# Optimization experiments

Measured on AMD Instinct MI355X. Metric: run time of the kernel, lower is better.

The kernel has to match this reference:

```python
import jax, jax.numpy as jnp
import numpy as np

N = 50000
E = 1600000
F = 128
G = 64  # number of graphs in the batch


def gat_layer(x, src, dst, W, a_src, a_dst, bias, heads, out_dim, concat):
    n = x.shape[0]
    h = (x @ W).reshape(n, heads, out_dim)                      # [N,H,D]
    alpha_src = jnp.sum(h * a_src, axis=-1)                     # [N,H]
    alpha_dst = jnp.sum(h * a_dst, axis=-1)                     # [N,H]
    e = jax.nn.leaky_relu(alpha_src[src] + alpha_dst[dst], negative_slope=0.2)  # [E,H]
    # segment softmax over edges grouped by destination node
    m = jax.ops.segment_max(e, dst, num_segments=n)
    m = jnp.where(jnp.isfinite(m), m, 0.0)
    ex = jnp.exp(e - m[dst])
    denom = jax.ops.segment_sum(ex, dst, num_segments=n)
    alpha = ex / (denom[dst] + 1e-16)                           # [E,H]
    msg = h[src] * alpha[:, :, None]                            # [E,H,D]
    out = jax.ops.segment_sum(msg, dst, num_segments=n)         # [N,H,D]
    if concat:
        out = out.reshape(n, heads * out_dim)
    else:
        out = out.mean(axis=1)
    return out + bias


def setup_inputs() -> dict:
    key = jax.random.key(0)
    ks = jax.random.split(key, 12)
    x = jax.random.normal(ks[0], (N, F), dtype=jnp.float32)
    edge_index = jax.random.randint(ks[1], (2, E), 0, N, dtype=jnp.int32)
    batch = jnp.sort(jax.random.randint(ks[2], (N,), 0, G, dtype=jnp.int32))
    s = 0.1
    W1 = jax.random.normal(ks[3], (F, 4 * 32), dtype=jnp.float32) * s
    a_src1 = jax.random.normal(ks[4], (4, 32), dtype=jnp.float32) * s
    a_dst1 = jax.random.normal(ks[5], (4, 32), dtype=jnp.float32) * s
    b1 = jnp.zeros((4 * 32,), dtype=jnp.float32)
    W2 = jax.random.normal(ks[6], (4 * 32, 2 * 16), dtype=jnp.float32) * s
    a_src2 = jax.random.normal(ks[7], (2, 16), dtype=jnp.float32) * s
    a_dst2 = jax.random.normal(ks[8], (2, 16), dtype=jnp.float32) * s
    b2 = jnp.zeros((16,), dtype=jnp.float32)
    fcW = jax.random.normal(ks[9], (16, 1), dtype=jnp.float32) * s
    fcb = jnp.zeros((1,), dtype=jnp.float32)
    return {"x": x, "edge_index": edge_index, "batch": batch,
            "W1": W1, "a_src1": a_src1, "a_dst1": a_dst1, "b1": b1,
            "W2": W2, "a_src2": a_src2, "a_dst2": a_dst2, "b2": b2,
            "fcW": fcW, "fcb": fcb}


def reference(x, edge_index, batch, W1, a_src1, a_dst1, b1, W2, a_src2, a_dst2, b2, fcW, fcb):
    n = x.shape[0]
    # PyG GATConv default: add self loops
    loops = jnp.arange(n, dtype=edge_index.dtype)
    src = jnp.concatenate([edge_index[0], loops])
    dst = jnp.concatenate([edge_index[1], loops])
    # eval mode: dropouts are no-ops
    h = jax.nn.relu(gat_layer(x, src, dst, W1, a_src1, a_dst1, b1, 4, 32, True))
    h = gat_layer(h, src, dst, W2, a_src2, a_dst2, b2, 2, 16, False)
    # global mean pool over graphs
    sums = jax.ops.segment_sum(h, batch, num_segments=G)        # [G,16]
    counts = jax.ops.segment_sum(jnp.ones((n,), h.dtype), batch, num_segments=G)
    pooled = sums / jnp.maximum(counts, 1.0)[:, None]
    return pooled @ fcW + fcb                                   # [G,1]
```

## Files before the change

kernel.cpp:

```cpp
#include <hip/hip_runtime.h>

#define LRELU(x) ((x) > 0.f ? (x) : 0.2f*(x))
typedef unsigned int uint;
typedef unsigned short ushort;
typedef _Float16 half2_t __attribute__((ext_vector_type(2)));

__device__ inline ushort f2bf(float f) {
    union { float f; unsigned u; } v; v.f = f;
    unsigned r = v.u + 0x7FFF + ((v.u >> 16) & 1);
    return (ushort)(r >> 16);
}
__device__ inline uint packbf(float a, float b) {
    return (uint)f2bf(a) | ((uint)f2bf(b) << 16);
}
__device__ inline float bflo(uint u){ union{uint u; float f;}v; v.u = u<<16; return v.f; }
__device__ inline float bfhi(uint u){ union{uint u; float f;}v; v.u = u & 0xFFFF0000u; return v.f; }
__device__ inline half2_t u2h(uint u){ union{uint u; half2_t h;}v; v.u=u; return v.h; }
__device__ inline uint h2u(half2_t h){ union{half2_t h; uint u;}v; v.h=h; return v.u; }
__device__ inline uint packh(float a, float b){
    half2_t h; h.x = (_Float16)a; h.y = (_Float16)b; return h2u(h);
}


#define CSR_SHIFT 7
#define CSR_NBLK  512

__global__ __launch_bounds__(256) void bucket_count_kernel(
    const int* __restrict__ dst, int E, int chunk, int nb,
    int* __restrict__ blockCntT)
{
    __shared__ int cnt[1024];
    int t = threadIdx.x, k = blockIdx.x;
    for (int i = t; i < nb; i += 256) cnt[i] = 0;
    __syncthreads();
    int e0 = k * chunk, e1 = min(e0 + chunk, E);
    for (int e = e0 + t * 4; e < e1; e += 1024) {
        int4 d4 = *(const int4*)(dst + e);
        atomicAdd(&cnt[d4.x >> CSR_SHIFT], 1);
        atomicAdd(&cnt[d4.y >> CSR_SHIFT], 1);
        atomicAdd(&cnt[d4.z >> CSR_SHIFT], 1);
        atomicAdd(&cnt[d4.w >> CSR_SHIFT], 1);
    }
    __syncthreads();
    for (int b = t; b < nb; b += 256)
        blockCntT[b * CSR_NBLK + k] = cnt[b];
}

__global__ __launch_bounds__(512) void row_scan_kernel(
    int* __restrict__ blockCntT, int* __restrict__ tot)
{
    __shared__ int sm[512];
    int b = blockIdx.x, t = threadIdx.x;
    int* row = blockCntT + b * CSR_NBLK;
    int v = row[t];
    sm[t] = v;
    __syncthreads();
    for (int off = 1; off < 512; off <<= 1) {
        int u = (t >= off) ? sm[t - off] : 0;
        __syncthreads(); sm[t] += u; __syncthreads();
    }
    row[t] = sm[t] - v;
    if (t == 511) tot[b] = sm[511];
}

__global__ __launch_bounds__(1024) void total_scan_kernel(
    const int* __restrict__ tot, int nb, int* __restrict__ bucketBase)
{
    __shared__ int sm[1024];
    int t = threadIdx.x;
    int v = (t < nb) ? tot[t] : 0;
    sm[t] = v;
    __syncthreads();
    for (int off = 1; off < 1024; off <<= 1) {
        int u = (t >= off) ? sm[t - off] : 0;
        __syncthreads(); sm[t] += u; __syncthreads();
    }
    if (t < nb) bucketBase[t] = sm[t] - v;
    if (t == 1023) bucketBase[nb] = sm[1023];
}

__global__ __launch_bounds__(256) void bucket_scatter_kernel(
    const int* __restrict__ src, const int* __restrict__ dst, int E, int chunk, int nb,
    const int* __restrict__ blockCntT, const int* __restrict__ bucketBase,
    uint* __restrict__ ebuf)
{
    __shared__ int cur[1024];
    int t = threadIdx.x, k = blockIdx.x;
    for (int b = t; b < nb; b += 256)
        cur[b] = bucketBase[b] + blockCntT[b * CSR_NBLK + k];
    __syncthreads();
    int e0 = k * chunk, e1 = min(e0 + chunk, E);
    for (int e = e0 + t * 4; e < e1; e += 1024) {
        int4 d4 = *(const int4*)(dst + e);
        int4 s4 = *(const int4*)(src + e);
        int p0 = atomicAdd(&cur[d4.x >> CSR_SHIFT], 1);
        ebuf[p0] = ((uint)s4.x << 7) | (uint)(d4.x & 127);
        int p1 = atomicAdd(&cur[d4.y >> CSR_SHIFT], 1);
        ebuf[p1] = ((uint)s4.y << 7) | (uint)(d4.y & 127);
        int p2 = atomicAdd(&cur[d4.z >> CSR_SHIFT], 1);
        ebuf[p2] = ((uint)s4.z << 7) | (uint)(d4.z & 127);
        int p3 = atomicAdd(&cur[d4.w >> CSR_SHIFT], 1);
        ebuf[p3] = ((uint)s4.w << 7) | (uint)(d4.w & 127);
    }
}

__global__ __launch_bounds__(256) void local_csr_kernel(
    const uint* __restrict__ ebuf, const int* __restrict__ bucketBase,
    int n, int E, int* __restrict__ rowptr, int* __restrict__ csr)
{
    __shared__ int lbase[1 << CSR_SHIFT];
    __shared__ int lcur[1 << CSR_SHIFT];
    __shared__ int ldeg[1 << CSR_SHIFT];
    int b = blockIdx.x, t = threadIdx.x;
    int n0 = b << CSR_SHIFT;
    int base = bucketBase[b], end = bucketBase[b + 1];
    if (t < (1 << CSR_SHIFT)) ldeg[t] = 0;
    __syncthreads();
    for (int e = base + t; e < end; e += 256)
        atomicAdd(&ldeg[ebuf[e] & 127], 1);
    __syncthreads();
    if (t == 0) {
        int run = base;
        for (int i = 0; i < (1 << CSR_SHIFT); ++i) {
            lbase[i] = run; lcur[i] = run; run += ldeg[i];
        }
    }
    __syncthreads();
    int node = n0 + t;
    if (t < (1 << CSR_SHIFT) && node < n) rowptr[node] = lbase[t];
    if (b == 0 && t == 0) rowptr[n] = E;
    for (int e = base + t; e < end; e += 256) {
        uint ed = ebuf[e];
        int pos = atomicAdd(&lcur[ed & 127], 1);
        csr[pos] = (int)(ed >> 7);
    }
}


template<int COLS, int HEADS, bool XBF16>
__global__ __launch_bounds__(256) void gemm_alpha_kernel(
    const void* __restrict__ xin, const float* __restrict__ W,
    const float* __restrict__ a_src, const float* __restrict__ a_dst,
    uint* __restrict__ hq, float* __restrict__ as_out,
    float* __restrict__ ad_out, int n)
{
    constexpr int K = 128;
    constexpr int K2 = K / 2;
    constexpr int CPT = COLS / 8;
    constexpr int NPT = 2;
    constexpr int DIM = COLS / HEADS;
    constexpr int TPH = DIM / CPT;
    constexpr int NSLOT4 = COLS / 4;
    __shared__ uint WLH[K2 * COLS];

    int t = threadIdx.x;
    for (int sid = t; sid < K2 * NSLOT4; sid += 256) {
        int k2 = sid / NSLOT4, s = sid % NSLOT4;
        int c = s * 4;
        float4 w0 = *(const float4*)(W + (2 * k2) * COLS + c);
        float4 w1 = *(const float4*)(W + (2 * k2 + 1) * COLS + c);
        uint4 u;
        u.x = packh(w0.x, w1.x);
        u.y = packh(w0.y, w1.y);
        u.z = packh(w0.z, w1.z);
        u.w = packh(w0.w, w1.w);
        int p = (COLS == 128) ? (((s & 3) << 3) | (s >> 2)) : s;
        ((uint4*)WLH)[k2 * NSLOT4 + p] = u;
    }
    __syncthreads();

    int m_ = t & 7;
    int node0 = blockIdx.x * (32 * NPT) + (t >> 3) * NPT;
    if (node0 >= n) return;
    int c0 = m_ * CPT;

    size_t rows[NPT];
#pragma unroll
    for (int i = 0; i < NPT; i++) rows[i] = (size_t)min(node0 + i, n - 1);

    float acc[NPT][CPT];
#pragma unroll
    for (int i = 0; i < NPT; i++)
#pragma unroll
        for (int q = 0; q < CPT; q++) acc[i][q] = 0.f;

    for (int k4 = 0; k4 < K; k4 += 4) {
        half2_t xp[NPT][2];
#pragma unroll
        for (int i = 0; i < NPT; i++) {
            if constexpr (XBF16) {
                uint2 u = *(const uint2*)((const uint*)xin + rows[i] * 64 + (k4 >> 1));
                half2_t h0; h0.x = (_Float16)bflo(u.x); h0.y = (_Float16)bfhi(u.x);
                half2_t h1; h1.x = (_Float16)bflo(u.y); h1.y = (_Float16)bfhi(u.y);
                xp[i][0] = h0; xp[i][1] = h1;
            } else {
                float4 v = *(const float4*)((const float*)xin + rows[i] * K + k4);
                half2_t h0; h0.x = (_Float16)v.x; h0.y = (_Float16)v.y;
                half2_t h1; h1.x = (_Float16)v.z; h1.y = (_Float16)v.w;
                xp[i][0] = h0; xp[i][1] = h1;
            }
        }
#pragma unroll
        for (int p = 0; p < 2; p++) {
            int k2 = (k4 >> 1) + p;
#pragma unroll
            for (int j = 0; j < CPT / 4; j++) {
                int slot = (COLS == 128) ? ((j << 3) | m_) : m_;
                uint4 wq = ((const uint4*)WLH)[k2 * NSLOT4 + slot];
                half2_t w0 = u2h(wq.x), w1 = u2h(wq.y), w2 = u2h(wq.z), w3 = u2h(wq.w);
#pragma unroll
                for (int i = 0; i < NPT; i++) {
                    half2_t xv = xp[i][p];
                    acc[i][j*4+0] = __builtin_amdgcn_fdot2(xv, w0, acc[i][j*4+0], false);
                    acc[i][j*4+1] = __builtin_amdgcn_fdot2(xv, w1, acc[i][j*4+1], false);
                    acc[i][j*4+2] = __builtin_amdgcn_fdot2(xv, w2, acc[i][j*4+2], false);
                    acc[i][j*4+3] = __builtin_amdgcn_fdot2(xv, w3, acc[i][j*4+3], false);
                }
            }
        }
    }

    int head = c0 / DIM, lc = c0 - head * DIM;
    float asc[CPT], adc[CPT];
#pragma unroll
    for (int q = 0; q < CPT; q++) {
        asc[q] = a_src[head * DIM + lc + q];
        adc[q] = a_dst[head * DIM + lc + q];
    }

#pragma unroll
    for (int i = 0; i < NPT; i++) {
        int node = node0 + i;
        if (node >= n) break;
        if constexpr (COLS == 128) {
            uint wds[4];
#pragma unroll
            for (int j = 0; j < 4; j++) {
                int u = 0;
                u = __builtin_amdgcn_cvt_pk_fp8_f32(acc[i][j*4+0], acc[i][j*4+1], u, false);
                u = __builtin_amdgcn_cvt_pk_fp8_f32(acc[i][j*4+2], acc[i][j*4+3], u, true);
                wds[j] = (uint)u;
            }
            *(uint4*)(hq + (size_t)node * 32 + m_ * 4) = make_uint4(wds[0], wds[1], wds[2], wds[3]);
        } else {
            int u = 0;
            u = __builtin_amdgcn_cvt_pk_fp8_f32(acc[i][0], acc[i][1], u, false);
            u = __builtin_amdgcn_cvt_pk_fp8_f32(acc[i][2], acc[i][3], u, true);
            hq[(size_t)node * 8 + m_] = (uint)u;
        }
        float ps = 0.f, pd = 0.f;
#pragma unroll
        for (int q = 0; q < CPT; q++) {
            ps += acc[i][q] * asc[q];
            pd += acc[i][q] * adc[q];
        }
#pragma unroll
        for (int off = 1; off < TPH; off <<= 1) {
            ps += __shfl_xor(ps, off);
            pd += __shfl_xor(pd, off);
        }
        if ((m_ & (TPH - 1)) == 0) {
            as_out[node * HEADS + head] = ps;
            ad_out[node * HEADS + head] = pd;
        }
    }
}


__global__ __launch_bounds__(256) void agg1_kernel(
    const float* __restrict__ as1f, const float* __restrict__ ad1f,
    const uint* __restrict__ h1q, const int* __restrict__ rowptr,
    const int* __restrict__ csr, const float* __restrict__ b1,
    uint* __restrict__ hrelu, int n)
{
    int t = threadIdx.x;
    int w = t >> 6, tw = t & 63;
    int g = tw >> 3, l = tw & 7;
    int head = l >> 1;
    int node = blockIdx.x * 4 + w;
    if (node >= n) return;

    float adh = ad1f[node * 4 + head];
    int rp = rowptr[node], re = rowptr[node + 1];

    float acc[16];
#pragma unroll
    for (int i = 0; i < 16; i++) acc[i] = 0.f;
    float den = 0.f;

#pragma unroll 2
    for (int e = rp + g; e < re; e += 8) {
        int s = csr[e];
        float a = as1f[s * 4 + head];
        uint4 u = *(const uint4*)(h1q + ((size_t)s << 5) + (l << 2));
        float ex = __expf(LRELU(a + adh));
        den += ex;
        uint ua[4] = {u.x, u.y, u.z, u.w};
#pragma unroll
        for (int j = 0; j < 4; j++) {
            auto p0 = __builtin_amdgcn_cvt_pk_f32_fp8(ua[j], false);
            auto p1 = __builtin_amdgcn_cvt_pk_f32_fp8(ua[j], true);
            acc[j*4+0] += ex * p0[0]; acc[j*4+1] += ex * p0[1];
            acc[j*4+2] += ex * p1[0]; acc[j*4+3] += ex * p1[1];
        }
    }

    if (g == 0) {
        float a = as1f[node * 4 + head];
        float ex = __expf(LRELU(a + adh));
        den += ex;
        uint4 u = *(const uint4*)(h1q + ((size_t)node << 5) + (l << 2));
        uint ua[4] = {u.x, u.y, u.z, u.w};
#pragma unroll
        for (int j = 0; j < 4; j++) {
            auto p0 = __builtin_amdgcn_cvt_pk_f32_fp8(ua[j], false);
            auto p1 = __builtin_amdgcn_cvt_pk_f32_fp8(ua[j], true);
            acc[j*4+0] += ex * p0[0]; acc[j*4+1] += ex * p0[1];
            acc[j*4+2] += ex * p1[0]; acc[j*4+3] += ex * p1[1];
        }
    }

#pragma unroll
    for (int i = 0; i < 16; i++) {
        acc[i] += __shfl_xor(acc[i], 8);
        acc[i] += __shfl_xor(acc[i], 16);
        acc[i] += __shfl_xor(acc[i], 32);
    }
    den += __shfl_xor(den, 8);
    den += __shfl_xor(den, 16);
    den += __shfl_xor(den, 32);

    if (g == 0) {
        float inv = 1.f / (den + 1e-16f);
        uint o[8];
#pragma unroll
        for (int j = 0; j < 4; j++) {
            float v0 = fmaxf(acc[j*4+0] * inv + b1[16*l + 4*j + 0], 0.f);
            float v1 = fmaxf(acc[j*4+1] * inv + b1[16*l + 4*j + 1], 0.f);
            float v2 = fmaxf(acc[j*4+2] * inv + b1[16*l + 4*j + 2], 0.f);
            float v3 = fmaxf(acc[j*4+3] * inv + b1[16*l + 4*j + 3], 0.f);
            o[2*j]   = packbf(v0, v1);
            o[2*j+1] = packbf(v2, v3);
        }
        uint* hp = hrelu + (size_t)node * 64 + l * 8;
        *(uint4*)hp       = make_uint4(o[0], o[1], o[2], o[3]);
        *(uint4*)(hp + 4) = make_uint4(o[4], o[5], o[6], o[7]);
    }
}


__global__ __launch_bounds__(256) void agg2_kernel(
    const float* __restrict__ as2f, const float* __restrict__ ad2f,
    const uint* __restrict__ h2q, const int* __restrict__ rowptr,
    const int* __restrict__ csr, const float* __restrict__ b2,
    float* __restrict__ hf, int n)
{
    int t = threadIdx.x;
    int w = t >> 6, tw = t & 63;
    int g = tw >> 3, l = tw & 7;
    int head = l >> 2;
    int node = blockIdx.x * 4 + w;
    if (node >= n) return;

    float adh = ad2f[node * 2 + head];
    int rp = rowptr[node], re = rowptr[node + 1];

    float acc[4] = {0.f, 0.f, 0.f, 0.f};
    float den = 0.f;

#pragma unroll 2
    for (int e = rp + g; e < re; e += 8) {
        int s = csr[e];
        float a = as2f[s * 2 + head];
        uint u = h2q[(size_t)s * 8 + l];
        float ex = __expf(LRELU(a + adh));
        den += ex;
        auto p0 = __builtin_amdgcn_cvt_pk_f32_fp8(u, false);
        auto p1 = __builtin_amdgcn_cvt_pk_f32_fp8(u, true);
        acc[0] += ex * p0[0]; acc[1] += ex * p0[1];
        acc[2] += ex * p1[0]; acc[3] += ex * p1[1];
    }

    if (g == 0) {
        float a = as2f[node * 2 + head];
        float ex = __expf(LRELU(a + adh));
        den += ex;
        uint u = h2q[(size_t)node * 8 + l];
        auto p0 = __builtin_amdgcn_cvt_pk_f32_fp8(u, false);
        auto p1 = __builtin_amdgcn_cvt_pk_f32_fp8(u, true);
        acc[0] += ex * p0[0]; acc[1] += ex * p0[1];
        acc[2] += ex * p1[0]; acc[3] += ex * p1[1];
    }

#pragma unroll
    for (int i = 0; i < 4; i++) {
        acc[i] += __shfl_xor(acc[i], 8);
        acc[i] += __shfl_xor(acc[i], 16);
        acc[i] += __shfl_xor(acc[i], 32);
    }
    den += __shfl_xor(den, 8);
    den += __shfl_xor(den, 16);
    den += __shfl_xor(den, 32);

    float inv = 1.f / (den + 1e-16f);
    float v0 = acc[0] * inv, v1 = acc[1] * inv, v2 = acc[2] * inv, v3 = acc[3] * inv;
    float o0 = 0.5f * (v0 + __shfl_xor(v0, 4));
    float o1 = 0.5f * (v1 + __shfl_xor(v1, 4));
    float o2 = 0.5f * (v2 + __shfl_xor(v2, 4));
    float o3 = 0.5f * (v3 + __shfl_xor(v3, 4));
    if (g == 0 && l < 4) {
        float4 o;
        o.x = o0 + b2[4*l+0]; o.y = o1 + b2[4*l+1];
        o.z = o2 + b2[4*l+2]; o.w = o3 + b2[4*l+3];
        *(float4*)(hf + (size_t)node * 16 + 4 * l) = o;
    }
}


__global__ __launch_bounds__(256) void pool_kernel(
    const float* __restrict__ hf, const int* __restrict__ batch,
    float* __restrict__ sums, float* __restrict__ counts, int n)
{
    int t = threadIdx.x;
    int d = t & 15, j = t >> 4;
    int base = blockIdx.x * 256 + j * 16;
    float run = 0.f, cnt = 0.f;
    int cg = -1;
    for (int i = 0; i < 16; ++i) {
        int nn = base + i;
        if (nn >= n) break;
        int g = batch[nn];
        if (g != cg) {
            if (cg >= 0) { atomicAdd(&sums[cg * 16 + d], run); if (d == 0) atomicAdd(&counts[cg], cnt); }
            cg = g; run = 0.f; cnt = 0.f;
        }
        run += hf[(size_t)nn * 16 + d];
        cnt += 1.f;
    }
    if (cg >= 0) { atomicAdd(&sums[cg * 16 + d], run); if (d == 0) atomicAdd(&counts[cg], cnt); }
}

__global__ void final_kernel(const float* __restrict__ sums, const float* __restrict__ counts,
                             const float* __restrict__ fcW, const float* __restrict__ fcb,
                             float* __restrict__ out, int G)
{
    int g = blockIdx.x * 64 + threadIdx.x;
    if (g < G) {
        float c = fmaxf(counts[g], 1.f);
        float s = 0.f;
        for (int dd = 0; dd < 16; ++dd) s += (sums[g * 16 + dd] / c) * fcW[dd];
        out[g] = s + fcb[0];
    }
}


extern "C" void kernel_launch(void* const* d_in, const int* in_sizes, int n_in,
                              void* d_out, int out_size, void* d_ws, size_t ws_size,
                              hipStream_t stream)
{
    const float* x      = (const float*)d_in[0];
    const int*   ei     = (const int*)d_in[1];
    const int*   batch  = (const int*)d_in[2];
    const float* W1     = (const float*)d_in[3];
    const float* a_src1 = (const float*)d_in[4];
    const float* a_dst1 = (const float*)d_in[5];
    const float* b1     = (const float*)d_in[6];
    const float* W2     = (const float*)d_in[7];
    const float* a_src2 = (const float*)d_in[8];
    const float* a_dst2 = (const float*)d_in[9];
    const float* b2     = (const float*)d_in[10];
    const float* fcW    = (const float*)d_in[11];
    const float* fcb    = (const float*)d_in[12];
    float* out = (float*)d_out;

    int n = in_sizes[0] / 128;
    int E = in_sizes[1] / 2;
    int G = out_size;
    const int* srcA = ei;
    const int* dstA = ei + E;

    int nb = (n + (1 << CSR_SHIFT) - 1) >> CSR_SHIFT;
    int chunk = (((E + CSR_NBLK - 1) / CSR_NBLK) + 3) & ~3;

    char* p = (char*)d_ws;
    auto alloc = [&](size_t bytes) { char* r = p; p += (bytes + 255) & ~(size_t)255; return r; };
    int*   blockCntT  = (int*)alloc((size_t)nb * CSR_NBLK * 4);
    int*   tot        = (int*)alloc((size_t)nb * 4);
    int*   bucketBase = (int*)alloc((size_t)(nb + 1) * 4);
    int*   rowptr     = (int*)alloc((size_t)(n + 1) * 4);
    int*   csr        = (int*)alloc((size_t)E * 4);
    uint*  h1q        = (uint*)alloc((size_t)n * 32 * 4);
    float* as1        = (float*)alloc((size_t)n * 16);
    float* ad1        = (float*)alloc((size_t)n * 16);
    uint*  hrelu      = (uint*)alloc((size_t)n * 64 * 4);
    uint*  h2q        = (uint*)alloc((size_t)n * 8 * 4);
    float* as2        = (float*)alloc((size_t)n * 8);
    float* ad2        = (float*)alloc((size_t)n * 8);
    float* hf         = (float*)alloc((size_t)n * 16 * 4);
    float* sums       = (float*)alloc((size_t)(G * 16 + G) * 4);
    float* counts     = sums + G * 16;

    uint* ebuf = (uint*)hrelu;

    hipMemsetAsync(sums, 0, (size_t)(G * 16 + G) * 4, stream);

    bucket_count_kernel<<<CSR_NBLK, 256, 0, stream>>>(dstA, E, chunk, nb, blockCntT);
    row_scan_kernel<<<nb, 512, 0, stream>>>(blockCntT, tot);
    total_scan_kernel<<<1, 1024, 0, stream>>>(tot, nb, bucketBase);
    bucket_scatter_kernel<<<CSR_NBLK, 256, 0, stream>>>(srcA, dstA, E, chunk, nb,
                                                        blockCntT, bucketBase, ebuf);
    local_csr_kernel<<<nb, 256, 0, stream>>>(ebuf, bucketBase, n, E, rowptr, csr);

    int gb = (n + 63) / 64;
    gemm_alpha_kernel<128, 4, false><<<gb, 256, 0, stream>>>(x, W1, a_src1, a_dst1,
                                                             h1q, as1, ad1, n);
    agg1_kernel<<<(n + 3) / 4, 256, 0, stream>>>(as1, ad1, h1q, rowptr, csr, b1, hrelu, n);
    gemm_alpha_kernel<32, 2, true><<<gb, 256, 0, stream>>>(hrelu, W2, a_src2, a_dst2,
                                                           h2q, as2, ad2, n);
    agg2_kernel<<<(n + 3) / 4, 256, 0, stream>>>(as2, ad2, h2q, rowptr, csr, b2, hf, n);
    pool_kernel<<<(n + 255) / 256, 256, 0, stream>>>(hf, batch, sums, counts, n);
    final_kernel<<<1, 64, 0, stream>>>(sums, counts, fcW, fcb, out, G);
}
```

Baseline: 183.4 us.

## Fuse layer-2 projection and attention logits into layer-1 aggregation epilogue

The layer-2 GEMM and its alpha computation move into the end of the layer-1 aggregation kernel. Each wave stages its node's ReLU output as fp16 in shared memory and dot-multiplies it against a packed fp16 copy of W2 held in LDS. It then writes the fp8 h2 and the as2/ad2 logits directly. This drops the bf16 hrelu intermediate write/read and one kernel launch, and the GEMM kernel is de-templated to its layer-1 form. In exchange, every 4-node block reloads and repacks W2 (16KB) into LDS, which adds per-block global/L2 traffic, a block-wide sync, and extra LDS use.

```diff
diff --git a/kernel.cpp b/kernel.cpp
--- a/kernel.cpp
+++ b/kernel.cpp
@@ -137,19 +137,17 @@
 }
 
 
-template<int COLS, int HEADS, bool XBF16>
 __global__ __launch_bounds__(256) void gemm_alpha_kernel(
-    const void* __restrict__ xin, const float* __restrict__ W,
+    const float* __restrict__ x, const float* __restrict__ W,
     const float* __restrict__ a_src, const float* __restrict__ a_dst,
     uint* __restrict__ hq, float* __restrict__ as_out,
     float* __restrict__ ad_out, int n)
 {
     constexpr int K = 128;
     constexpr int K2 = K / 2;
-    constexpr int CPT = COLS / 8;
+    constexpr int COLS = 128;
+    constexpr int CPT = 16;
     constexpr int NPT = 2;
-    constexpr int DIM = COLS / HEADS;
-    constexpr int TPH = DIM / CPT;
     constexpr int NSLOT4 = COLS / 4;
     __shared__ uint WLH[K2 * COLS];
 
@@ -164,7 +162,7 @@
         u.y = packh(w0.y, w1.y);
         u.z = packh(w0.z, w1.z);
         u.w = packh(w0.w, w1.w);
-        int p = (COLS == 128) ? (((s & 3) << 3) | (s >> 2)) : s;
+        int p = ((s & 3) << 3) | (s >> 2);
         ((uint4*)WLH)[k2 * NSLOT4 + p] = u;
     }
     __syncthreads();
@@ -188,24 +186,17 @@
         half2_t xp[NPT][2];
 #pragma unroll
         for (int i = 0; i < NPT; i++) {
-            if constexpr (XBF16) {
-                uint2 u = *(const uint2*)((const uint*)xin + rows[i] * 64 + (k4 >> 1));
-                half2_t h0; h0.x = (_Float16)bflo(u.x); h0.y = (_Float16)bfhi(u.x);
-                half2_t h1; h1.x = (_Float16)bflo(u.y); h1.y = (_Float16)bfhi(u.y);
-                xp[i][0] = h0; xp[i][1] = h1;
-            } else {
-                float4 v = *(const float4*)((const float*)xin + rows[i] * K + k4);
-                half2_t h0; h0.x = (_Float16)v.x; h0.y = (_Float16)v.y;
-                half2_t h1; h1.x = (_Float16)v.z; h1.y = (_Float16)v.w;
-                xp[i][0] = h0; xp[i][1] = h1;
-            }
+            float4 v = *(const float4*)(x + rows[i] * K + k4);
+            half2_t h0; h0.x = (_Float16)v.x; h0.y = (_Float16)v.y;
+            half2_t h1; h1.x = (_Float16)v.z; h1.y = (_Float16)v.w;
+            xp[i][0] = h0; xp[i][1] = h1;
         }
 #pragma unroll
         for (int p = 0; p < 2; p++) {
             int k2 = (k4 >> 1) + p;
 #pragma unroll
-            for (int j = 0; j < CPT / 4; j++) {
-                int slot = (COLS == 128) ? ((j << 3) | m_) : m_;
+            for (int j = 0; j < 4; j++) {
+                int slot = (j << 3) | m_;
                 uint4 wq = ((const uint4*)WLH)[k2 * NSLOT4 + slot];
                 half2_t w0 = u2h(wq.x), w1 = u2h(wq.y), w2 = u2h(wq.z), w3 = u2h(wq.w);
 #pragma unroll
@@ -220,60 +211,61 @@
         }
     }
 
-    int head = c0 / DIM, lc = c0 - head * DIM;
+    int head = c0 / 32, lc = c0 - head * 32;
     float asc[CPT], adc[CPT];
 #pragma unroll
     for (int q = 0; q < CPT; q++) {
-        asc[q] = a_src[head * DIM + lc + q];
-        adc[q] = a_dst[head * DIM + lc + q];
+        asc[q] = a_src[head * 32 + lc + q];
+        adc[q] = a_dst[head * 32 + lc + q];
     }
 
 #pragma unroll
     for (int i = 0; i < NPT; i++) {
         int node = node0 + i;
         if (node >= n) break;
-        if constexpr (COLS == 128) {
-            uint wds[4];
-#pragma unroll
-            for (int j = 0; j < 4; j++) {
-                int u = 0;
-                u = __builtin_amdgcn_cvt_pk_fp8_f32(acc[i][j*4+0], acc[i][j*4+1], u, false);
-                u = __builtin_amdgcn_cvt_pk_fp8_f32(acc[i][j*4+2], acc[i][j*4+3], u, true);
-                wds[j] = (uint)u;
-            }
-            *(uint4*)(hq + (size_t)node * 32 + m_ * 4) = make_uint4(wds[0], wds[1], wds[2], wds[3]);
-        } else {
+        uint wds[4];
+#pragma unroll
+        for (int j = 0; j < 4; j++) {
             int u = 0;
-            u = __builtin_amdgcn_cvt_pk_fp8_f32(acc[i][0], acc[i][1], u, false);
-            u = __builtin_amdgcn_cvt_pk_fp8_f32(acc[i][2], acc[i][3], u, true);
-            hq[(size_t)node * 8 + m_] = (uint)u;
-        }
+            u = __builtin_amdgcn_cvt_pk_fp8_f32(acc[i][j*4+0], acc[i][j*4+1], u, false);
+            u = __builtin_amdgcn_cvt_pk_fp8_f32(acc[i][j*4+2], acc[i][j*4+3], u, true);
+            wds[j] = (uint)u;
+        }
+        *(uint4*)(hq + (size_t)node * 32 + m_ * 4) = make_uint4(wds[0], wds[1], wds[2], wds[3]);
         float ps = 0.f, pd = 0.f;
 #pragma unroll
         for (int q = 0; q < CPT; q++) {
             ps += acc[i][q] * asc[q];
             pd += acc[i][q] * adc[q];
         }
-#pragma unroll
-        for (int off = 1; off < TPH; off <<= 1) {
-            ps += __shfl_xor(ps, off);
-            pd += __shfl_xor(pd, off);
-        }
-        if ((m_ & (TPH - 1)) == 0) {
-            as_out[node * HEADS + head] = ps;
-            ad_out[node * HEADS + head] = pd;
-        }
-    }
-}
-
-
-__global__ __launch_bounds__(256) void agg1_kernel(
+        ps += __shfl_xor(ps, 1);
+        pd += __shfl_xor(pd, 1);
+        if ((m_ & 1) == 0) {
+            as_out[node * 4 + head] = ps;
+            ad_out[node * 4 + head] = pd;
+        }
+    }
+}
+
+
+__global__ __launch_bounds__(256) void agg1_fused_kernel(
     const float* __restrict__ as1f, const float* __restrict__ ad1f,
     const uint* __restrict__ h1q, const int* __restrict__ rowptr,
     const int* __restrict__ csr, const float* __restrict__ b1,
-    uint* __restrict__ hrelu, int n)
-{
+    const float* __restrict__ W2, const float* __restrict__ a_src2,
+    const float* __restrict__ a_dst2,
+    uint* __restrict__ h2q, float* __restrict__ as2, float* __restrict__ ad2, int n)
+{
+    __shared__ uint W2L[64 * 32];
+    __shared__ uint HL[4][64];
+
     int t = threadIdx.x;
+    for (int idx = t; idx < 64 * 32; idx += 256) {
+        int k2 = idx >> 5, col = idx & 31;
+        W2L[idx] = packh(W2[(2 * k2) * 32 + col], W2[(2 * k2 + 1) * 32 + col]);
+    }
+    __syncthreads();
+
     int w = t >> 6, tw = t & 63;
     int g = tw >> 3, l = tw & 7;
     int head = l >> 1;
@@ -330,21 +322,47 @@
     den += __shfl_xor(den, 16);
     den += __shfl_xor(den, 32);
 
+    float inv = 1.f / (den + 1e-16f);
     if (g == 0) {
-        float inv = 1.f / (den + 1e-16f);
-        uint o[8];
-#pragma unroll
-        for (int j = 0; j < 4; j++) {
-            float v0 = fmaxf(acc[j*4+0] * inv + b1[16*l + 4*j + 0], 0.f);
-            float v1 = fmaxf(acc[j*4+1] * inv + b1[16*l + 4*j + 1], 0.f);
-            float v2 = fmaxf(acc[j*4+2] * inv + b1[16*l + 4*j + 2], 0.f);
-            float v3 = fmaxf(acc[j*4+3] * inv + b1[16*l + 4*j + 3], 0.f);
-            o[2*j]   = packbf(v0, v1);
-            o[2*j+1] = packbf(v2, v3);
-        }
-        uint* hp = hrelu + (size_t)node * 64 + l * 8;
-        *(uint4*)hp       = make_uint4(o[0], o[1], o[2], o[3]);
-        *(uint4*)(hp + 4) = make_uint4(o[4], o[5], o[6], o[7]);
+#pragma unroll
+        for (int j = 0; j < 8; j++) {
+            float v0 = fmaxf(acc[2*j+0] * inv + b1[16*l + 2*j + 0], 0.f);
+            float v1 = fmaxf(acc[2*j+1] * inv + b1[16*l + 2*j + 1], 0.f);
+            HL[w][8*l + j] = packh(v0, v1);
+        }
+    }
+    __builtin_amdgcn_wave_barrier();
+
+    int col = tw & 31, kh = tw >> 5;
+    float s2 = 0.f;
+#pragma unroll
+    for (int k2i = 0; k2i < 32; k2i++) {
+        int k2 = kh * 32 + k2i;
+        s2 = __builtin_amdgcn_fdot2(u2h(HL[w][k2]), u2h(W2L[k2 * 32 + col]), s2, false);
+    }
+    s2 += __shfl_xor(s2, 32);
+
+    int h2head = col >> 4, lc = col & 15;
+    float ps = s2 * a_src2[h2head * 16 + lc];
+    float pd = s2 * a_dst2[h2head * 16 + lc];
+    ps += __shfl_xor(ps, 1); pd += __shfl_xor(pd, 1);
+    ps += __shfl_xor(ps, 2); pd += __shfl_xor(pd, 2);
+    ps += __shfl_xor(ps, 4); pd += __shfl_xor(pd, 4);
+    ps += __shfl_xor(ps, 8); pd += __shfl_xor(pd, 8);
+    if (tw < 32 && lc == 0) {
+        as2[node * 2 + h2head] = ps;
+        ad2[node * 2 + h2head] = pd;
+    }
+
+    float a0 = __shfl(s2, (tw & 7) * 4 + 0);
+    float a1 = __shfl(s2, (tw & 7) * 4 + 1);
+    float a2 = __shfl(s2, (tw & 7) * 4 + 2);
+    float a3 = __shfl(s2, (tw & 7) * 4 + 3);
+    if (tw < 8) {
+        int u = 0;
+        u = __builtin_amdgcn_cvt_pk_fp8_f32(a0, a1, u, false);
+        u = __builtin_amdgcn_cvt_pk_fp8_f32(a2, a3, u, true);
+        h2q[(size_t)node * 8 + tw] = (uint)u;
     }
 }
 
@@ -489,10 +507,10 @@
     int*   bucketBase = (int*)alloc((size_t)(nb + 1) * 4);
     int*   rowptr     = (int*)alloc((size_t)(n + 1) * 4);
     int*   csr        = (int*)alloc((size_t)E * 4);
+    uint*  ebuf       = (uint*)alloc((size_t)E * 4);
     uint*  h1q        = (uint*)alloc((size_t)n * 32 * 4);
     float* as1        = (float*)alloc((size_t)n * 16);
     float* ad1        = (float*)alloc((size_t)n * 16);
-    uint*  hrelu      = (uint*)alloc((size_t)n * 64 * 4);
     uint*  h2q        = (uint*)alloc((size_t)n * 8 * 4);
     float* as2        = (float*)alloc((size_t)n * 8);
     float* ad2        = (float*)alloc((size_t)n * 8);
@@ -500,8 +518,6 @@
     float* sums       = (float*)alloc((size_t)(G * 16 + G) * 4);
     float* counts     = sums + G * 16;
 
-    uint* ebuf = (uint*)hrelu;
-
     hipMemsetAsync(sums, 0, (size_t)(G * 16 + G) * 4, stream);
 
     bucket_count_kernel<<<CSR_NBLK, 256, 0, stream>>>(dstA, E, chunk, nb, blockCntT);
@@ -512,11 +528,10 @@
     local_csr_kernel<<<nb, 256, 0, stream>>>(ebuf, bucketBase, n, E, rowptr, csr);
 
     int gb = (n + 63) / 64;
-    gemm_alpha_kernel<128, 4, false><<<gb, 256, 0, stream>>>(x, W1, a_src1, a_dst1,
-                                                             h1q, as1, ad1, n);
-    agg1_kernel<<<(n + 3) / 4, 256, 0, stream>>>(as1, ad1, h1q, rowptr, csr, b1, hrelu, n);
-    gemm_alpha_kernel<32, 2, true><<<gb, 256, 0, stream>>>(hrelu, W2, a_src2, a_dst2,
-                                                           h2q, as2, ad2, n);
+    gemm_alpha_kernel<<<gb, 256, 0, stream>>>(x, W1, a_src1, a_dst1, h1q, as1, ad1, n);
+    agg1_fused_kernel<<<(n + 3) / 4, 256, 0, stream>>>(as1, ad1, h1q, rowptr, csr, b1,
+                                                       W2, a_src2, a_dst2,
+                                                       h2q, as2, ad2, n);
     agg2_kernel<<<(n + 3) / 4, 256, 0, stream>>>(as2, ad2, h2q, rowptr, csr, b2, hf, n);
     pool_kernel<<<(n + 255) / 256, 256, 0, stream>>>(hf, batch, sums, counts, n);
     final_kernel<<<1, 64, 0, stream>>>(sums, counts, fcW, fcb, out, G);
```

New measurement: 194.5 us. +6.1%, slower.
